# Performance work log

Measured on AMD Instinct MI355X. Metric: run time of the kernel, lower is better.

## Reference

```python
import jax, jax.numpy as jnp
import numpy as np

N_HEADS = 8
TOP_K = 100


def setup_inputs() -> dict:
    key = jax.random.key(0)
    ks = jax.random.split(key, 12)
    B, S, H, U = 16, 2048, 1024, 512
    s = 0.02
    return {
        "query": jax.random.normal(ks[0], (B, H), jnp.float32),
        "values": jax.random.normal(ks[1], (B, S, H), jnp.float32),
        # stacked per-head Bahdanau params (8 heads)
        "W1": jax.random.normal(ks[2], (N_HEADS, H, U), jnp.float32) * s,
        "b1": jnp.zeros((N_HEADS, U), jnp.float32),
        "W2": jax.random.normal(ks[3], (N_HEADS, H, U), jnp.float32) * s,
        "b2": jnp.zeros((N_HEADS, U), jnp.float32),
        "Vw": jax.random.normal(ks[4], (N_HEADS, U), jnp.float32) * s,
        "Vb": jnp.zeros((N_HEADS,), jnp.float32),
        # head-mixing linear W: nbr_heads -> 1
        "Ww": jax.random.normal(ks[5], (N_HEADS,), jnp.float32) * s,
        "Wb": jnp.zeros((), jnp.float32),
    }


def reference(query, values, W1, b1, W2, b2, Vw, Vb, Ww, Wb):
    # per-head additive attention scores, vectorized over the 8 heads
    # values: [B,S,H], query: [B,H]
    hid = jnp.tanh(
        jnp.einsum('bsh,nhu->nbsu', values, W1) + b1[:, None, None, :]
        + jnp.einsum('bh,nhu->nbu', query, W2)[:, :, None, :] + b2[:, None, None, :]
    )  # [N,B,S,U]
    scores = jnp.einsum('nbsu,nu->bsn', hid, Vw) + Vb  # [B,S,N] == concat of 8 head scores
    score = jnp.einsum('bsn,n->bs', scores, Ww) + Wb   # [B,S]

    # topk over sequence dim, then zero all non-topk positions:
    # torch: score = -(score.scatter(1, top_pos, 0) - score)
    _, top_pos = jax.lax.top_k(score, TOP_K)           # [B,K]
    bidx = jnp.arange(score.shape[0])[:, None]
    sc0 = score.at[bidx, top_pos].set(0.0)
    masked = (score - sc0)[..., None]                  # [B,S,1]: topk vals kept, 0 else

    # custom sigmoid 'softmax' normalized over the BATCH dim (dim 0), as in source
    w = jax.nn.sigmoid(masked)
    w = w / w.sum(0)                                   # [B,S,1]
    context = (w * values).sum(1)                      # [B,H]
    return context, w, masked
```

## Files before the change

kernel.cpp:

```cpp
#include <hip/hip_runtime.h>
#include <hip/hip_bf16.h>

#define B_ 16
#define S_ 2048
#define H_ 1024
#define U_ 512
#define NH 8
#define TOPK 100

#define M_ (B_*S_)
#define NC (NH*U_)

typedef int i32x4 __attribute__((ext_vector_type(4)));

__device__ __forceinline__ float fast_tanh(float x) {
    float e = __expf(2.f * x);
    return (e - 1.f) / (e + 1.f);
}

__device__ __forceinline__ void gl16i(const signed char* g, signed char* l) {
    __builtin_amdgcn_global_load_lds(
        (const __attribute__((address_space(1))) void*)g,
        (__attribute__((address_space(3))) void*)l, 16, 0, 0);
}

__global__ void cvtA(const float* __restrict__ v,
                     signed char* __restrict__ h8,
                     float* __restrict__ sa) {
    int row = blockIdx.x * 4 + (threadIdx.x >> 6);
    int l = threadIdx.x & 63;
    const float4* r4 = (const float4*)(v + (size_t)row * 1024);
    float4 x[4];
    float mx = 0.f;
    #pragma unroll
    for (int c = 0; c < 4; ++c) {
        x[c] = r4[l * 4 + c];
        mx = fmaxf(mx, fmaxf(fmaxf(fabsf(x[c].x), fabsf(x[c].y)),
                             fmaxf(fabsf(x[c].z), fabsf(x[c].w))));
    }
    #pragma unroll
    for (int d = 1; d < 64; d <<= 1) mx = fmaxf(mx, __shfl_xor(mx, d));
    float inv = 127.f / mx;
    int wh[4];
    #pragma unroll
    for (int c = 0; c < 4; ++c) {
        float xs[4] = {x[c].x, x[c].y, x[c].z, x[c].w};
        unsigned ph = 0;
        #pragma unroll
        for (int j = 0; j < 4; ++j) {
            float hf = rintf(xs[j] * inv);
            ph |= ((unsigned)((int)hf) & 0xffu) << (8 * j);
        }
        wh[c] = (int)ph;
    }
    *(int4*)(h8 + (size_t)row * 1024 + l * 16) = make_int4(wh[0], wh[1], wh[2], wh[3]);
    if (l == 0) sa[row] = mx / 127.f;
}

__global__ void colmax_kernel(const float* __restrict__ W1, float* __restrict__ cm) {
    int n = blockIdx.x, h0 = blockIdx.y * 64, u = threadIdx.x;
    const float* p = W1 + ((size_t)n * H_ + h0) * U_ + u;
    float mx = 0.f;
    #pragma unroll 8
    for (int h = 0; h < 64; ++h) mx = fmaxf(mx, fabsf(p[(size_t)h * U_]));
    atomicMax((unsigned*)(cm + n * U_ + u), __float_as_uint(mx));
}

__global__ void cvtB8(const float* __restrict__ W1,
                      const float* __restrict__ cm,
                      signed char* __restrict__ bh) {
    __shared__ float t[64][65];
    int n = blockIdx.x, h0 = blockIdx.y * 64, u0 = blockIdx.z * 64;
    int tid = threadIdx.x;
    int ul = tid & 63;
    #pragma unroll
    for (int i = 0; i < 16; ++i) {
        int hl = i * 4 + (tid >> 6);
        t[hl][ul] = W1[((size_t)n * H_ + h0 + hl) * U_ + u0 + ul];
    }
    __syncthreads();
    #pragma unroll
    for (int i = 0; i < 16; ++i) {
        int ulw = i * 4 + (tid >> 6);
        int hlw = tid & 63;
        float q = t[hlw][ulw] * (127.f / cm[n * 512 + u0 + ulw]);
        size_t o = ((size_t)(n * 512 + u0 + ulw)) * 1024 + h0 + hlw;
        bh[o] = (signed char)(int)rintf(q);
    }
}

__global__ void qbp_kernel(const float* __restrict__ query,
                           const float* __restrict__ W2,
                           float* __restrict__ qbp) {
    int n = blockIdx.x, hc = blockIdx.y;
    int u = threadIdx.x;
    int h0 = hc * 64;
    __shared__ float q[16][64];
    #pragma unroll
    for (int k = 0; k < 2; ++k) {
        int idx = threadIdx.x + k * 512;
        q[idx >> 6][idx & 63] = query[(idx >> 6) * H_ + h0 + (idx & 63)];
    }
    __syncthreads();
    float acc[16];
    #pragma unroll
    for (int b = 0; b < 16; ++b) acc[b] = 0.f;
    const float* w2 = W2 + ((size_t)n * H_ + h0) * U_ + u;
    #pragma unroll 4
    for (int hh = 0; hh < 64; ++hh) {
        float wv = w2[(size_t)hh * U_];
        #pragma unroll
        for (int b = 0; b < 16; ++b) acc[b] = fmaf(q[b][hh], wv, acc[b]);
    }
    float* dst = qbp + ((size_t)hc * NH + n) * 16 * U_ + u;
    #pragma unroll
    for (int b = 0; b < 16; ++b) dst[(size_t)b * U_] = acc[b];
}

__global__ void qb_reduce(const float* __restrict__ qbp,
                          const float* __restrict__ b1,
                          const float* __restrict__ b2,
                          float* __restrict__ qb) {
    int i = blockIdx.x * 256 + threadIdx.x;
    int n = i >> 13;
    int u = i & 511;
    float s = b1[n * U_ + u] + b2[n * U_ + u];
    #pragma unroll
    for (int hc = 0; hc < 16; ++hc) s += qbp[(size_t)hc * 65536 + i];
    qb[i] = s;
}

#define NT 16
#define SWZ(d) ((d) ^ ((((d) >> 7) & 3) << 4))
#define K0B(tt) ((tt) * 64)
#define STAGE_A(tt, j) gl16i(Ah8 + (size_t)(rowBase + (j)*128 + rT) * 1024 + K0B(tt) + cTb, \
                             lds + ((tt)&1)*32768 + (j)*8192 + tid*16)
#define STAGE_B(tt, j) gl16i(Bh8 + (size_t)(colBase + (j)*128 + rT) * 1024 + K0B(tt) + cTb, \
                             lds + ((tt)&1)*32768 + 16384 + (j)*8192 + tid*16)

__global__ __launch_bounds__(512, 2) void gemm8i(
        const signed char* __restrict__ Ah8,
        const signed char* __restrict__ Bh8,
        const float* __restrict__ sa, const float* __restrict__ cm,
        const float* __restrict__ qb, const float* __restrict__ Vw,
        const float* __restrict__ Ww, float* __restrict__ partial) {
    __shared__ signed char lds[65536];
    const int tid = threadIdx.x;
    const int lane = tid & 63;
    const int wid = tid >> 6;
    const int wm = wid >> 2, wn = wid & 3;
    int bid = blockIdx.x;
    int swz = (bid & 7) * 256 + (bid >> 3);
    int mIdx = swz & 127, nIdx = swz >> 7;
    int rowBase = mIdx * 256, colBase = nIdx * 256;

    int d0 = tid * 16;
    int d0s = SWZ(d0);
    int rT  = d0s >> 6;
    int cTb = d0s & 63;

    const int l15 = lane & 15, l4 = lane >> 4;
    int offA[8], offB[4];
    #pragma unroll
    for (int m = 0; m < 8; ++m)
        offA[m] = SWZ((wm * 128 + m * 16 + l15) * 64 + l4 * 16);
    #pragma unroll
    for (int n = 0; n < 4; ++n)
        offB[n] = 16384 + SWZ((wn * 64 + n * 16 + l15) * 64 + l4 * 16);

    i32x4 acc[8][4];
    #pragma unroll
    for (int m = 0; m < 8; ++m)
        #pragma unroll
        for (int n = 0; n < 4; ++n) acc[m][n] = (i32x4){0, 0, 0, 0};

    STAGE_A(0, 0); STAGE_A(0, 1); STAGE_B(0, 0); STAGE_B(0, 1);
    asm volatile("s_waitcnt vmcnt(0)" ::: "memory");
    __builtin_amdgcn_s_barrier();

    #pragma unroll 1
    for (int t = 0; t < NT; ++t) {
        __builtin_amdgcn_sched_barrier(0);
        if (t + 1 < NT) {
            STAGE_A(t + 1, 0); STAGE_A(t + 1, 1);
            STAGE_B(t + 1, 0); STAGE_B(t + 1, 1);
        }
        const signed char* slot = lds + (t & 1) * 32768;
        i32x4 bf[4], af[8];
        #pragma unroll
        for (int n = 0; n < 4; ++n) bf[n] = *(const i32x4*)(slot + offB[n]);
        #pragma unroll
        for (int m = 0; m < 8; ++m) af[m] = *(const i32x4*)(slot + offA[m]);
        #pragma unroll
        for (int m = 0; m < 8; ++m)
            #pragma unroll
            for (int n = 0; n < 4; ++n)
                acc[m][n] = __builtin_amdgcn_mfma_i32_16x16x64_i8(af[m], bf[n], acc[m][n], 0, 0, 0);
        asm volatile("s_waitcnt lgkmcnt(0)" ::: "memory");
        asm volatile("s_waitcnt vmcnt(0)" ::: "memory");
        __builtin_amdgcn_s_barrier();
    }

    int hd = colBase >> 9;
    int b = rowBase >> 11;
    float wwn = Ww[hd];
    float qv[4], vw[4], sbv[4];
    #pragma unroll
    for (int n = 0; n < 4; ++n) {
        int col = colBase + wn * 64 + n * 16 + l15;
        int u = col & 511;
        qv[n] = qb[((size_t)hd * B_ + b) * U_ + u];
        vw[n] = Vw[hd * U_ + u] * wwn;
        sbv[n] = cm[col] * (1.f / 127.f);
    }
    float* red = (float*)lds;
    #pragma unroll
    for (int m = 0; m < 8; ++m) {
        float sav[4];
        #pragma unroll
        for (int r = 0; r < 4; ++r)
            sav[r] = sa[rowBase + wm * 128 + m * 16 + l4 * 4 + r];
        #pragma unroll
        for (int r = 0; r < 4; ++r) {
            float p = 0.f;
            #pragma unroll
            for (int n = 0; n < 4; ++n)
                p += vw[n] * fast_tanh((float)acc[m][n][r] * sav[r] * sbv[n] + qv[n]);
            p += __shfl_xor(p, 1);
            p += __shfl_xor(p, 2);
            p += __shfl_xor(p, 4);
            p += __shfl_xor(p, 8);
            if (l15 == 0)
                red[wn * 256 + wm * 128 + m * 16 + l4 * 4 + r] = p;
        }
    }
    __syncthreads();
    if (tid < 256) {
        float s = red[tid] + red[256 + tid] + red[512 + tid] + red[768 + tid];
        partial[(size_t)nIdx * M_ + rowBase + tid] = s;
    }
}

__global__ __launch_bounds__(256, 2) void gemm_score(
        const float* __restrict__ values,
        const float* __restrict__ W1,
        const float* __restrict__ qb,
        const float* __restrict__ Vw,
        const float* __restrict__ Ww,
        float* __restrict__ partial) {
    __shared__ float As[16][128 + 4];
    __shared__ float Bs[16][128 + 4];
    int tid = threadIdx.x;
    int tx = tid & 15, ty = tid >> 4;
    int rowBase = blockIdx.x * 128;
    int colBase = blockIdx.y * 128;
    int n = colBase >> 9;
    int u0 = colBase & 511;
    int b = rowBase >> 11;
    float acc[8][8];
    #pragma unroll
    for (int i = 0; i < 8; ++i)
        #pragma unroll
        for (int j = 0; j < 8; ++j) acc[i][j] = 0.f;
    const float* Ag = values + (size_t)rowBase * H_;
    const float* Bg = W1 + (size_t)n * H_ * U_ + u0;
    for (int k0 = 0; k0 < H_; k0 += 16) {
        #pragma unroll
        for (int r = 0; r < 2; ++r) {
            int idx = tid + r * 256;
            int arow = idx >> 2, aqc = idx & 3;
            float4 v = *(const float4*)(Ag + (size_t)arow * H_ + k0 + aqc * 4);
            As[aqc * 4 + 0][arow] = v.x;
            As[aqc * 4 + 1][arow] = v.y;
            As[aqc * 4 + 2][arow] = v.z;
            As[aqc * 4 + 3][arow] = v.w;
        }
        #pragma unroll
        for (int r = 0; r < 2; ++r) {
            int idx = tid + r * 256;
            int bk = idx >> 5, bqc = idx & 31;
            float4 v = *(const float4*)(Bg + (size_t)(k0 + bk) * U_ + bqc * 4);
            *(float4*)&Bs[bk][bqc * 4] = v;
        }
        __syncthreads();
        #pragma unroll
        for (int k = 0; k < 16; ++k) {
            float4 a0 = *(const float4*)&As[k][ty * 8];
            float4 a1 = *(const float4*)&As[k][ty * 8 + 4];
            float4 b0 = *(const float4*)&Bs[k][tx * 8];
            float4 b1v = *(const float4*)&Bs[k][tx * 8 + 4];
            float av[8] = {a0.x, a0.y, a0.z, a0.w, a1.x, a1.y, a1.z, a1.w};
            float bv[8] = {b0.x, b0.y, b0.z, b0.w, b1v.x, b1v.y, b1v.z, b1v.w};
            #pragma unroll
            for (int i = 0; i < 8; ++i)
                #pragma unroll
                for (int j = 0; j < 8; ++j)
                    acc[i][j] = fmaf(av[i], bv[j], acc[i][j]);
        }
        __syncthreads();
    }
    float qbv[8], vwv[8];
    #pragma unroll
    for (int j = 0; j < 8; ++j) {
        int u = u0 + tx * 8 + j;
        qbv[j] = qb[(n * B_ + b) * U_ + u];
        vwv[j] = Vw[n * U_ + u];
    }
    float wwn = Ww[n];
    #pragma unroll
    for (int i = 0; i < 8; ++i) {
        float p = 0.f;
        #pragma unroll
        for (int j = 0; j < 8; ++j)
            p += vwv[j] * fast_tanh(acc[i][j] + qbv[j]);
        p += __shfl_xor(p, 1);
        p += __shfl_xor(p, 2);
        p += __shfl_xor(p, 4);
        p += __shfl_xor(p, 8);
        if (tx == 0)
            partial[(size_t)blockIdx.y * M_ + rowBase + ty * 8 + i] = wwn * p;
    }
}

__global__ __launch_bounds__(1024) void topk_kernel(
        const float* __restrict__ partial, int nparts,
        const float* __restrict__ Vb,
        const float* __restrict__ Ww,
        const float* __restrict__ Wb,
        float* __restrict__ out_masked,
        float* __restrict__ w_un) {
    __shared__ float sc[S_];
    __shared__ float srt[S_];
    __shared__ int cnt_gt;
    int b = blockIdx.x;
    int tid = threadIdx.x;
    float cst = Wb[0];
    #pragma unroll
    for (int n2 = 0; n2 < NH; ++n2) cst += Ww[n2] * Vb[n2];
    for (int s = tid; s < S_; s += 1024) {
        float v = cst;
        for (int ct = 0; ct < nparts; ++ct)
            v += partial[(size_t)ct * M_ + b * S_ + s];
        sc[s] = v; srt[s] = v;
    }
    if (tid == 0) cnt_gt = 0;
    __syncthreads();
    for (int k = 2; k <= S_; k <<= 1) {
        for (int j = k >> 1; j >= 1; j >>= 1) {
            int i = ((tid & ~(j - 1)) << 1) | (tid & (j - 1));
            int p = i | j;
            float a = srt[i], c2 = srt[p];
            if (((i & k) == 0) ? (a > c2) : (a < c2)) { srt[i] = c2; srt[p] = a; }
            __syncthreads();
        }
    }
    float T = srt[S_ - TOPK];
    int c = 0;
    for (int s = tid; s < S_; s += 1024) c += (sc[s] > T);
    atomicAdd(&cnt_gt, c);
    __syncthreads();
    int need_eq = TOPK - cnt_gt;
    for (int s = tid; s < S_; s += 1024) {
        float v = sc[s];
        bool sel = (v > T);
        if (v == T) {
            int rank = 0;
            for (int t2 = 0; t2 < s; ++t2) rank += (sc[t2] == T);
            sel = (rank < need_eq);
        }
        float m = sel ? v : 0.f;
        out_masked[b * S_ + s] = m;
        w_un[b * S_ + s] = 1.f / (1.f + __expf(-m));
    }
}

__global__ void norm_w(const float* __restrict__ w_un, float* __restrict__ out_w) {
    int s = blockIdx.x * blockDim.x + threadIdx.x;
    float d = 0.f;
    #pragma unroll
    for (int b = 0; b < B_; ++b) d += w_un[b * S_ + s];
    float inv = 1.f / d;
    #pragma unroll
    for (int b = 0; b < B_; ++b) out_w[b * S_ + s] = w_un[b * S_ + s] * inv;
}

__global__ void ctx_partial_h8(const signed char* __restrict__ h8,
                               const float* __restrict__ sa,
                               const float* __restrict__ w,
                               float* __restrict__ pctx) {
    int bb = blockIdx.x;
    int h = blockIdx.y * 256 + threadIdx.x;
    int s0 = blockIdx.z * 256;
    __shared__ float ws[256];
    {
        int s = threadIdx.x;
        ws[s] = w[bb * S_ + s0 + s] * sa[bb * S_ + s0 + s];
    }
    __syncthreads();
    const signed char* hp = h8 + (size_t)(bb * S_ + s0) * H_ + h;
    float acc = 0.f;
    #pragma unroll 4
    for (int s = 0; s < 256; ++s)
        acc += ws[s] * (float)hp[(size_t)s * H_];
    pctx[((size_t)blockIdx.z * B_ + bb) * H_ + h] = acc;
}

__global__ void ctx_partial_f32(const float* __restrict__ values,
                                const float* __restrict__ w,
                                float* __restrict__ pctx) {
    int bb = blockIdx.x;
    int h = blockIdx.y * 256 + threadIdx.x;
    int s0 = blockIdx.z * 256;
    __shared__ float wrow[256];
    wrow[threadIdx.x] = w[bb * S_ + s0 + threadIdx.x];
    __syncthreads();
    const float* vp = values + (size_t)(bb * S_ + s0) * H_ + h;
    float acc = 0.f;
    #pragma unroll 4
    for (int s = 0; s < 256; ++s) acc += wrow[s] * vp[(size_t)s * H_];
    pctx[((size_t)blockIdx.z * B_ + bb) * H_ + h] = acc;
}

__global__ void ctx_reduce(const float* __restrict__ pctx,
                           float* __restrict__ out_ctx) {
    int i = blockIdx.x * blockDim.x + threadIdx.x;
    float s = 0.f;
    #pragma unroll
    for (int z = 0; z < 8; ++z) s += pctx[(size_t)z * B_ * H_ + i];
    out_ctx[i] = s;
}

extern "C" void kernel_launch(void* const* d_in, const int* in_sizes, int n_in,
                              void* d_out, int out_size, void* d_ws, size_t ws_size,
                              hipStream_t stream) {
    const float* query = (const float*)d_in[0];
    const float* values = (const float*)d_in[1];
    const float* W1 = (const float*)d_in[2];
    const float* b1 = (const float*)d_in[3];
    const float* W2 = (const float*)d_in[4];
    const float* b2 = (const float*)d_in[5];
    const float* Vw = (const float*)d_in[6];
    const float* Vb = (const float*)d_in[7];
    const float* Ww = (const float*)d_in[8];
    const float* Wb = (const float*)d_in[9];

    float* ws = (float*)d_ws;
    float* qb      = ws;
    float* qbp     = qb + 65536;
    float* partial = qbp + 1048576;
    float* w_un    = partial + 1048576;
    float* pctx    = w_un + 32768;
    float* sa      = pctx + 131072;
    float* colmax  = sa + 32768;
    signed char* Ah8 = (signed char*)(colmax + 4096);
    signed char* Bh8 = Ah8 + (size_t)M_ * H_;
    size_t needed = (size_t)((char*)(Bh8 + (size_t)NC * H_) - (char*)d_ws);

    float* out_ctx    = (float*)d_out;
    float* out_w      = out_ctx + 16384;
    float* out_masked = out_w + 32768;

    qbp_kernel<<<dim3(NH, 16), 512, 0, stream>>>(query, W2, qbp);
    qb_reduce<<<dim3(256), 256, 0, stream>>>(qbp, b1, b2, qb);
    if (ws_size >= needed) {
        cvtA<<<dim3(8192), 256, 0, stream>>>(values, Ah8, sa);
        hipMemsetAsync(colmax, 0, NC * sizeof(float), stream);
        colmax_kernel<<<dim3(NH, 16), 512, 0, stream>>>(W1, colmax);
        cvtB8<<<dim3(NH, 16, 8), 256, 0, stream>>>(W1, colmax, Bh8);
        gemm8i<<<dim3(2048), 512, 0, stream>>>(Ah8, Bh8, sa, colmax,
                                               qb, Vw, Ww, partial);
        topk_kernel<<<16, 1024, 0, stream>>>(partial, 16, Vb, Ww, Wb, out_masked, w_un);
        norm_w<<<8, 256, 0, stream>>>(w_un, out_w);
        ctx_partial_h8<<<dim3(16, 4, 8), 256, 0, stream>>>(Ah8, sa, out_w, pctx);
    } else {
        gemm_score<<<dim3(256, 32), 256, 0, stream>>>(values, W1, qb, Vw, Ww, partial);
        topk_kernel<<<16, 1024, 0, stream>>>(partial, 32, Vb, Ww, Wb, out_masked, w_un);
        norm_w<<<8, 256, 0, stream>>>(w_un, out_w);
        ctx_partial_f32<<<dim3(16, 4, 8), 256, 0, stream>>>(values, out_w, pctx);
    }
    ctx_reduce<<<64, 256, 0, stream>>>(pctx, out_ctx);
}
```

Baseline: 394.7 us.

## Replace bitonic sort with radix select for top-k threshold; vectorize int8 context loads

The top-k kernel no longer runs a full bitonic sort of 2048 scores with many block barriers. Instead it maps each float to an order-preserving unsigned key and runs a 4-pass, 8-bit radix select with shared-memory histograms to find the k-th largest value. Tie handling downstream is unchanged. Separately, the int8 context partial kernel now loads 4 bytes per thread and keeps four accumulators, so each block covers all of H with a smaller grid.

After: 405.1 us. 1.03x slower.

```diff
diff --git a/kernel.cpp b/kernel.cpp
--- a/kernel.cpp
+++ b/kernel.cpp
@@ -330,7 +330,10 @@
         float* __restrict__ out_masked,
         float* __restrict__ w_un) {
     __shared__ float sc[S_];
-    __shared__ float srt[S_];
+    __shared__ unsigned ou[S_];
+    __shared__ unsigned hist[256];
+    __shared__ unsigned sel_pref;
+    __shared__ unsigned sel_rank;
     __shared__ int cnt_gt;
     int b = blockIdx.x;
     int tid = threadIdx.x;
@@ -341,20 +344,39 @@
         float v = cst;
         for (int ct = 0; ct < nparts; ++ct)
             v += partial[(size_t)ct * M_ + b * S_ + s];
-        sc[s] = v; srt[s] = v;
-    }
-    if (tid == 0) cnt_gt = 0;
-    __syncthreads();
-    for (int k = 2; k <= S_; k <<= 1) {
-        for (int j = k >> 1; j >= 1; j >>= 1) {
-            int i = ((tid & ~(j - 1)) << 1) | (tid & (j - 1));
-            int p = i | j;
-            float a = srt[i], c2 = srt[p];
-            if (((i & k) == 0) ? (a > c2) : (a < c2)) { srt[i] = c2; srt[p] = a; }
-            __syncthreads();
-        }
-    }
-    float T = srt[S_ - TOPK];
+        sc[s] = v;
+        unsigned u = __float_as_uint(v);
+        ou[s] = ((int)u >= 0) ? (u | 0x80000000u) : ~u;
+    }
+    if (tid == 0) { sel_pref = 0u; sel_rank = TOPK; cnt_gt = 0; }
+    __syncthreads();
+    #pragma unroll
+    for (int shift = 24; shift >= 0; shift -= 8) {
+        if (tid < 256) hist[tid] = 0;
+        __syncthreads();
+        unsigned pref = sel_pref;
+        unsigned mhi = (shift == 24) ? 0u : (0xFFFFFFFFu << (shift + 8));
+        for (int s = tid; s < S_; s += 1024) {
+            unsigned u = ou[s];
+            if ((u & mhi) == pref) atomicAdd(&hist[(u >> shift) & 255u], 1u);
+        }
+        __syncthreads();
+        if (tid == 0) {
+            unsigned r = sel_rank;
+            int byte = 255;
+            for (; byte > 0; --byte) {
+                unsigned c = hist[byte];
+                if (r <= c) break;
+                r -= c;
+            }
+            sel_rank = r;
+            sel_pref = pref | ((unsigned)byte << shift);
+        }
+        __syncthreads();
+    }
+    unsigned Tou = sel_pref;
+    unsigned fb = (Tou & 0x80000000u) ? (Tou & 0x7FFFFFFFu) : ~Tou;
+    float T = __uint_as_float(fb);
     int c = 0;
     for (int s = tid; s < S_; s += 1024) c += (sc[s] > T);
     atomicAdd(&cnt_gt, c);
@@ -389,20 +411,24 @@
                                const float* __restrict__ w,
                                float* __restrict__ pctx) {
     int bb = blockIdx.x;
-    int h = blockIdx.y * 256 + threadIdx.x;
-    int s0 = blockIdx.z * 256;
+    int s0 = blockIdx.y * 256;
+    int h4 = threadIdx.x * 4;
     __shared__ float ws[256];
-    {
-        int s = threadIdx.x;
-        ws[s] = w[bb * S_ + s0 + s] * sa[bb * S_ + s0 + s];
-    }
-    __syncthreads();
-    const signed char* hp = h8 + (size_t)(bb * S_ + s0) * H_ + h;
-    float acc = 0.f;
+    ws[threadIdx.x] = w[bb * S_ + s0 + threadIdx.x] * sa[bb * S_ + s0 + threadIdx.x];
+    __syncthreads();
+    const signed char* hp = h8 + (size_t)(bb * S_ + s0) * H_ + h4;
+    float a0 = 0.f, a1 = 0.f, a2 = 0.f, a3 = 0.f;
     #pragma unroll 4
-    for (int s = 0; s < 256; ++s)
-        acc += ws[s] * (float)hp[(size_t)s * H_];
-    pctx[((size_t)blockIdx.z * B_ + bb) * H_ + h] = acc;
+    for (int s = 0; s < 256; ++s) {
+        int v = *(const int*)(hp + (size_t)s * H_);
+        float wv = ws[s];
+        a0 = fmaf(wv, (float)(signed char)(v), a0);
+        a1 = fmaf(wv, (float)(signed char)(v >> 8), a1);
+        a2 = fmaf(wv, (float)(signed char)(v >> 16), a2);
+        a3 = fmaf(wv, (float)(v >> 24), a3);
+    }
+    float* dst = pctx + ((size_t)blockIdx.y * B_ + bb) * H_ + h4;
+    dst[0] = a0; dst[1] = a1; dst[2] = a2; dst[3] = a3;
 }
 
 __global__ void ctx_partial_f32(const float* __restrict__ values,
@@ -471,7 +497,7 @@
                                                qb, Vw, Ww, partial);
         topk_kernel<<<16, 1024, 0, stream>>>(partial, 16, Vb, Ww, Wb, out_masked, w_un);
         norm_w<<<8, 256, 0, stream>>>(w_un, out_w);
-        ctx_partial_h8<<<dim3(16, 4, 8), 256, 0, stream>>>(Ah8, sa, out_w, pctx);
+        ctx_partial_h8<<<dim3(16, 8), 256, 0, stream>>>(Ah8, sa, out_w, pctx);
     } else {
         gemm_score<<<dim3(256, 32), 256, 0, stream>>>(values, W1, qb, Vw, Ww, partial);
         topk_kernel<<<16, 1024, 0, stream>>>(partial, 32, Vb, Ww, Wb, out_masked, w_un);
```
